# Performance work log

Measured on AMD Instinct MI355X. Metric: run time of the kernel, lower is better.

Reference implementation:

```python
import jax, jax.numpy as jnp
import numpy as np


def setup_inputs() -> dict:
    key = jax.random.key(0)
    ks = jax.random.split(key, 5)
    B, S, D = 4, 2048, 768
    scale = 0.02  # keep pre-softmax scores in a sane range
    return {
        "x": jax.random.normal(ks[0], (B, S, D), dtype=jnp.float32),
        "wq": jax.random.normal(ks[1], (D, D), dtype=jnp.float32) * scale,
        "wk": jax.random.normal(ks[2], (D, D), dtype=jnp.float32) * scale,
        "wv": jax.random.normal(ks[3], (D, D), dtype=jnp.float32) * scale,
        "wo": jax.random.normal(ks[4], (D, D), dtype=jnp.float32) * scale,
    }


NUM_HEADS = 12
NEG = -1000000000.0


def reference(x, wq, wk, wv, wo):
    B, S, D = x.shape
    H = NUM_HEADS
    dh = D // H
    # nn.Linear(bias=False): y = x @ W.T ; split heads -> [B, H, S, dh]
    def proj(w):
        return (x @ w.T).reshape(B, S, H, dh).transpose(0, 2, 1, 3)
    q, k, v = proj(wq), proj(wk), proj(wv)
    # scores [B, H, S, S] with causal mask (strict upper triangle gets -1e9 added)
    score = jnp.einsum("bhqd,bhkd->bhqk", q, k) / jnp.float32(np.sqrt(dh))
    causal = jnp.triu(jnp.ones((S, S), dtype=bool), k=1)
    score = score + jnp.where(causal, jnp.float32(NEG), jnp.float32(0.0))
    attn = jax.nn.softmax(score, axis=-1)
    out = jnp.einsum("bhqk,bhkd->bhqd", attn, v)
    out = out.transpose(0, 2, 1, 3).reshape(B, S, D)
    return out @ wo.T
```

## Files before the change

### kernel.cpp

```cpp
#include <hip/hip_runtime.h>
#include <stdint.h>

typedef unsigned short u16;
typedef __attribute__((ext_vector_type(8))) short short8;
typedef __attribute__((ext_vector_type(4))) short s16x4;
typedef __attribute__((ext_vector_type(4))) float f32x4;
typedef __attribute__((ext_vector_type(2))) unsigned uint2v;

#define MFMA16(a, b, c) __builtin_amdgcn_mfma_f32_16x16x32_bf16(a, b, c, 0, 0, 0)

#if __has_builtin(__builtin_amdgcn_mfma_f32_16x16x16bf16_1k)
__device__ __forceinline__ f32x4 pv_mfma(s16x4 a, s16x4 b, f32x4 c) {
  return __builtin_amdgcn_mfma_f32_16x16x16bf16_1k(a, b, c, 0, 0, 0);
}
#else
__device__ __forceinline__ f32x4 pv_mfma(s16x4 a, s16x4 b, f32x4 c) {
  asm volatile("v_mfma_f32_16x16x16_bf16 %0, %1, %2, %0" : "+v"(c) : "v"(a), "v"(b));
  return c;
}
#endif

__device__ __forceinline__ void async16(void* lds, const void* g) {
  __builtin_amdgcn_global_load_lds(
      (const __attribute__((address_space(1))) void*)g,
      (__attribute__((address_space(3))) void*)lds, 16, 0, 0);
}

__device__ __forceinline__ u16 f2bf(float f) {
  unsigned u = __float_as_uint(f);
  u += 0x7FFF + ((u >> 16) & 1);
  return (u16)(u >> 16);
}

__device__ __forceinline__ unsigned cvtpk(float lo, float hi) {
  unsigned r;
  asm("v_cvt_pk_bf16_f32 %0, %1, %2" : "=v"(r) : "v"(lo), "v"(hi));
  return r;
}

#define QSCALE 0.18033688011112042f
#define MASKV -30000.0f

__global__ void convert_x(const float* __restrict__ src, u16* __restrict__ dst) {
  int i = blockIdx.x * 256 + threadIdx.x;
  float4 v = ((const float4*)src)[i];
  unsigned lo = (unsigned)f2bf(v.x) | ((unsigned)f2bf(v.y) << 16);
  unsigned hi = (unsigned)f2bf(v.z) | ((unsigned)f2bf(v.w) << 16);
  ((uint2*)dst)[i] = make_uint2(lo, hi);
}

__global__ void convert_w(const float* __restrict__ wq, const float* __restrict__ wk,
                          const float* __restrict__ wv, const float* __restrict__ wo,
                          u16* __restrict__ wqkv, u16* __restrict__ wob) {
  int i = blockIdx.x * 256 + threadIdx.x;
  int wsel = i / 147456;
  int r = i - wsel * 147456;
  const float* s = (wsel == 0) ? wq : (wsel == 1) ? wk : (wsel == 2) ? wv : wo;
  float4 v = ((const float4*)s)[r];
  unsigned lo = (unsigned)f2bf(v.x) | ((unsigned)f2bf(v.y) << 16);
  unsigned hi = (unsigned)f2bf(v.z) | ((unsigned)f2bf(v.w) << 16);
  uint2 w = make_uint2(lo, hi);
  if (wsel < 3) ((uint2*)wqkv)[wsel * 147456 + r] = w;
  else ((uint2*)wob)[r] = w;
}

template <int MODE>
__global__ __launch_bounds__(256) void gemm_bt(const u16* __restrict__ A,
                                               const u16* __restrict__ Bw,
                                               u16* __restrict__ Qb, u16* __restrict__ Kb,
                                               u16* __restrict__ Vb, float* __restrict__ Out) {
  __shared__ __align__(16) u16 As[128 * 32];
  __shared__ __align__(16) u16 Bs[128 * 32];
  const int bm = blockIdx.x & 63;
  const int bn = blockIdx.x >> 6;
  const int tid = threadIdx.x;
  const int wave = tid >> 6, lane = tid & 63;
  const int arow = lane & 15, kg = lane >> 4;
  const int wr = wave >> 1, wc = wave & 1;

  const int o = tid * 16;
  const int rowS = o >> 6;
  const int cbS = o & 63;
  const char* gA0 = (const char*)A + (size_t)(bm * 128 + rowS) * 1536 + cbS;
  const char* gA1 = gA0 + (size_t)64 * 1536;
  const char* gB0 = (const char*)Bw + (size_t)(bn * 128 + rowS) * 1536 + cbS;
  const char* gB1 = gB0 + (size_t)64 * 1536;
  char* lA = (char*)As + wave * 1024;
  char* lB = (char*)Bs + wave * 1024;

  f32x4 acc[4][4];
#pragma unroll
  for (int m = 0; m < 4; ++m)
#pragma unroll
    for (int n = 0; n < 4; ++n) acc[m][n] = (f32x4)(0.0f);

  for (int kk = 0; kk < 24; ++kk) {
    async16(lA, gA0);
    async16(lA + 4096, gA1);
    async16(lB, gB0);
    async16(lB + 4096, gB1);
    gA0 += 64; gA1 += 64; gB0 += 64; gB1 += 64;
    __syncthreads();
    short8 av[4], bv[4];
#pragma unroll
    for (int m = 0; m < 4; ++m)
      av[m] = *(const short8*)(As + (wr * 64 + m * 16 + arow) * 32 + kg * 8);
#pragma unroll
    for (int n = 0; n < 4; ++n)
      bv[n] = *(const short8*)(Bs + (wc * 64 + n * 16 + arow) * 32 + kg * 8);
#pragma unroll
    for (int m = 0; m < 4; ++m)
#pragma unroll
      for (int n = 0; n < 4; ++n) acc[m][n] = MFMA16(av[m], bv[n], acc[m][n]);
    __syncthreads();
  }

#pragma unroll
  for (int m = 0; m < 4; ++m) {
    const int rbase = bm * 128 + wr * 64 + m * 16 + kg * 4;
#pragma unroll
    for (int n = 0; n < 4; ++n) {
      const int c = bn * 128 + wc * 64 + n * 16 + arow;
#pragma unroll
      for (int i = 0; i < 4; ++i) {
        float v = acc[m][n][i];
        int rr = rbase + i;
        if (MODE == 0) {
          int which = c / 768;
          int hc = c - which * 768;
          int h = hc >> 6, d = hc & 63;
          int b = rr >> 11, s = rr & 2047;
          size_t bh = (size_t)(b * 12 + h);
          if (which == 0) {
            Qb[(bh * 2048 + s) * 64 + d] = f2bf(v * QSCALE);
          } else if (which == 1) {
            Kb[(bh * 2048 + s) * 64 + d] = f2bf(v);
          } else {
            Vb[(bh * 64 + d) * 2048 + s] = f2bf(v);
          }
        } else {
          Out[(size_t)rr * 768 + c] = v;
        }
      }
    }
  }
}

__global__ __launch_bounds__(256) void attn_kernel(const u16* __restrict__ Qb,
                                                   const u16* __restrict__ Kb,
                                                   const u16* __restrict__ Vb,
                                                   u16* __restrict__ AOb) {
  __shared__ __align__(16) u16 Ks[2][64 * 64];
  __shared__ __align__(16) u16 Vt[2][64 * 64];

  const int bid = blockIdx.x;
  const int qt = 31 - (bid / 48);
  const int bh = bid % 48;
  const int tid = threadIdx.x, wave = tid >> 6, lane = tid & 63;
  const int arow = lane & 15, kg = lane >> 4;
  const size_t hbase = (size_t)bh * (2048 * 64);
  const u16* Qh = Qb + hbase;
  const int q0 = qt * 64 + wave * 16;

  short8 qf[2];
#pragma unroll
  for (int ks = 0; ks < 2; ++ks)
    qf[ks] = *(const short8*)(Qh + (size_t)(q0 + arow) * 64 + ks * 32 + kg * 8);

  f32x4 o_acc[4];
#pragma unroll
  for (int n = 0; n < 4; ++n) o_acc[n] = (f32x4)(0.0f);
  float mrow = MASKV, lrow = 0.0f;

  const int o0 = tid * 16;
  const int r0 = o0 >> 7, cb0 = o0 & 127;
  const int r1 = r0 + 32;
  const int sw0 = cb0 ^ (((r0 ^ (r0 >> 3)) & 7) << 4);
  const int sw1 = cb0 ^ (((r1 ^ (r1 >> 3)) & 7) << 4);
  char* const KsB = (char*)Ks;
  char* const VtB = (char*)Vt;
  const int ldsw = wave * 1024;

  const char* gK0 = (const char*)(Kb + hbase) + r0 * 128 + sw0;
  const char* gK1 = (const char*)(Kb + hbase) + r1 * 128 + sw1;
  const char* gV0 = (const char*)(Vb + hbase) + (size_t)r0 * 4096 + sw0;
  const char* gV1 = (const char*)(Vb + hbase) + (size_t)r1 * 4096 + sw1;

  const int ktiles = qt + 1;

  auto stage = [&](int buf) {
    async16(KsB + buf * 8192 + ldsw,        gK0);
    async16(KsB + buf * 8192 + ldsw + 4096, gK1);
    async16(VtB + buf * 8192 + ldsw,        gV0);
    async16(VtB + buf * 8192 + ldsw + 4096, gV1);
    gK0 += 8192; gK1 += 8192; gV0 += 128; gV1 += 128;
  };

  stage(0);
  asm volatile("s_waitcnt vmcnt(0)" ::: "memory");
  __builtin_amdgcn_s_barrier();

  int cur = 0;
  for (int kt = 0; kt < ktiles; ++kt) {
    if (kt + 1 < ktiles) stage(cur ^ 1);

    const char* Kc = KsB + cur * 8192;
    const char* Vc = VtB + cur * 8192;

    f32x4 s_acc[4];
#pragma unroll
    for (int cg = 0; cg < 4; ++cg) s_acc[cg] = (f32x4)(0.0f);
#pragma unroll
    for (int cg = 0; cg < 4; ++cg) {
      int krow = cg * 16 + arow;
      int fsw = ((krow ^ (krow >> 3)) & 7) << 4;
#pragma unroll
      for (int ks = 0; ks < 2; ++ks) {
        short8 kf = *(const short8*)(Kc + (krow << 7) + ((ks * 64 + kg * 16) ^ fsw));
        s_acc[cg] = MFMA16(kf, qf[ks], s_acc[cg]);
      }
    }

    if (kt == ktiles - 1) {
      int rel = wave * 16 + arow - kg * 4;
#pragma unroll
      for (int cg = 0; cg < 4; ++cg)
#pragma unroll
        for (int i = 0; i < 4; ++i)
          s_acc[cg][i] = (cg * 16 + i > rel) ? MASKV : s_acc[cg][i];
    }

    float rmax = s_acc[0][0];
#pragma unroll
    for (int cg = 0; cg < 4; ++cg)
#pragma unroll
      for (int i = 0; i < 4; ++i) rmax = fmaxf(rmax, s_acc[cg][i]);
    rmax = fmaxf(rmax, __shfl_xor(rmax, 16));
    rmax = fmaxf(rmax, __shfl_xor(rmax, 32));

    {
      float mnew = fmaxf(mrow, rmax);
      float corr = exp2f(mrow - mnew);
      mrow = mnew;
      lrow *= corr;
#pragma unroll
      for (int n = 0; n < 4; ++n)
#pragma unroll
        for (int i = 0; i < 4; ++i) o_acc[n][i] *= corr;
    }

    float p[4][4];
    float rs = 0.0f;
#pragma unroll
    for (int cg = 0; cg < 4; ++cg)
#pragma unroll
      for (int i = 0; i < 4; ++i) {
        float e = exp2f(s_acc[cg][i] - mrow);
        p[cg][i] = e;
        rs += e;
      }
    rs += __shfl_xor(rs, 16);
    rs += __shfl_xor(rs, 32);
    lrow += rs;

    s16x4 pb[4];
#pragma unroll
    for (int cg = 0; cg < 4; ++cg) {
      uint2v w;
      w.x = cvtpk(p[cg][0], p[cg][1]);
      w.y = cvtpk(p[cg][2], p[cg][3]);
      pb[cg] = __builtin_bit_cast(s16x4, w);
    }

#pragma unroll
    for (int n = 0; n < 4; ++n) {
      int vrow = n * 16 + arow;
      int f2 = ((vrow ^ (vrow >> 3)) & 7) << 4;
      const char* vb0 = Vc + (vrow << 7);
#pragma unroll
      for (int cg = 0; cg < 4; ++cg) {
        s16x4 va = *(const s16x4*)(vb0 + ((cg * 32 + kg * 8) ^ f2));
        o_acc[n] = pv_mfma(va, pb[cg], o_acc[n]);
      }
    }

    asm volatile("s_waitcnt vmcnt(0)" ::: "memory");
    __builtin_amdgcn_s_barrier();
    cur ^= 1;
  }

  const int b = bh / 12, h = bh - b * 12;
  float rinv = 1.0f / lrow;
  size_t obase = ((size_t)b * 2048 + q0 + arow) * 768 + h * 64 + kg * 4;
#pragma unroll
  for (int n = 0; n < 4; ++n) {
#pragma unroll
    for (int t = 0; t < 2; ++t) {
      unsigned w = cvtpk(o_acc[n][2 * t] * rinv, o_acc[n][2 * t + 1] * rinv);
      *(unsigned*)(&AOb[obase + n * 16 + 2 * t]) = w;
    }
  }
}

extern "C" void kernel_launch(void* const* d_in, const int* in_sizes, int n_in,
                              void* d_out, int out_size, void* d_ws, size_t ws_size,
                              hipStream_t stream) {
  const float* x = (const float*)d_in[0];
  const float* wq = (const float*)d_in[1];
  const float* wk = (const float*)d_in[2];
  const float* wv = (const float*)d_in[3];
  const float* wo = (const float*)d_in[4];
  float* out = (float*)d_out;

  char* ws = (char*)d_ws;
  u16* xb   = (u16*)(ws);
  u16* wqkv = (u16*)(ws + 12582912);
  u16* wob  = (u16*)(ws + 16121856);
  u16* Qb   = (u16*)(ws + 17301504);
  u16* Kb   = (u16*)(ws + 29884416);
  u16* Vb   = (u16*)(ws + 42467328);
  u16* AOb  = (u16*)(ws + 55050240);

  convert_x<<<6144, 256, 0, stream>>>(x, xb);
  convert_w<<<2304, 256, 0, stream>>>(wq, wk, wv, wo, wqkv, wob);

  gemm_bt<0><<<64 * 18, 256, 0, stream>>>(xb, wqkv, Qb, Kb, Vb, nullptr);
  attn_kernel<<<48 * 32, 256, 0, stream>>>(Qb, Kb, Vb, AOb);
  gemm_bt<1><<<64 * 6, 256, 0, stream>>>(AOb, wob, nullptr, nullptr, nullptr, out);
}
```

Before: 153.1 us.

## Double-buffer GEMM LDS tiles and vectorize the transposed V epilogue stores

The QKV and output GEMMs now use two LDS buffers, so the async global-to-LDS load of the next K-slice is issued before the MFMAs on the current slice run. This overlaps memory latency with compute and leaves one barrier per iteration instead of two. The epilogue is also restructured: per-block values (head, which matrix) are hoisted, and the transposed V output is packed two bf16 at a time into 8-byte stores instead of scattered scalar writes. The cost is doubled LDS per block, which may reduce occupancy, and a vmcnt(0) wait that still stalls on each stage.

```diff
diff --git a/kernel.cpp b/kernel.cpp
--- a/kernel.cpp
+++ b/kernel.cpp
@@ -69,8 +69,8 @@
                                                const u16* __restrict__ Bw,
                                                u16* __restrict__ Qb, u16* __restrict__ Kb,
                                                u16* __restrict__ Vb, float* __restrict__ Out) {
-  __shared__ __align__(16) u16 As[128 * 32];
-  __shared__ __align__(16) u16 Bs[128 * 32];
+  __shared__ __align__(16) u16 As[2][128 * 32];
+  __shared__ __align__(16) u16 Bs[2][128 * 32];
   const int bm = blockIdx.x & 63;
   const int bn = blockIdx.x >> 6;
   const int tid = threadIdx.x;
@@ -85,8 +85,7 @@
   const char* gA1 = gA0 + (size_t)64 * 1536;
   const char* gB0 = (const char*)Bw + (size_t)(bn * 128 + rowS) * 1536 + cbS;
   const char* gB1 = gB0 + (size_t)64 * 1536;
-  char* lA = (char*)As + wave * 1024;
-  char* lB = (char*)Bs + wave * 1024;
+  const int ldsw = wave * 1024;
 
   f32x4 acc[4][4];
 #pragma unroll
@@ -94,55 +93,84 @@
 #pragma unroll
     for (int n = 0; n < 4; ++n) acc[m][n] = (f32x4)(0.0f);
 
+  auto stage = [&](int buf) {
+    async16((char*)As + buf * 8192 + ldsw,        gA0);
+    async16((char*)As + buf * 8192 + ldsw + 4096, gA1);
+    async16((char*)Bs + buf * 8192 + ldsw,        gB0);
+    async16((char*)Bs + buf * 8192 + ldsw + 4096, gB1);
+    gA0 += 64; gA1 += 64; gB0 += 64; gB1 += 64;
+  };
+
+  stage(0);
+  asm volatile("s_waitcnt vmcnt(0)" ::: "memory");
+  __builtin_amdgcn_s_barrier();
+
+  int cur = 0;
   for (int kk = 0; kk < 24; ++kk) {
-    async16(lA, gA0);
-    async16(lA + 4096, gA1);
-    async16(lB, gB0);
-    async16(lB + 4096, gB1);
-    gA0 += 64; gA1 += 64; gB0 += 64; gB1 += 64;
-    __syncthreads();
+    if (kk + 1 < 24) stage(cur ^ 1);
+
+    const char* Ac = (const char*)As + cur * 8192;
+    const char* Bc = (const char*)Bs + cur * 8192;
     short8 av[4], bv[4];
 #pragma unroll
     for (int m = 0; m < 4; ++m)
-      av[m] = *(const short8*)(As + (wr * 64 + m * 16 + arow) * 32 + kg * 8);
+      av[m] = *(const short8*)(Ac + (wr * 64 + m * 16 + arow) * 64 + kg * 16);
 #pragma unroll
     for (int n = 0; n < 4; ++n)
-      bv[n] = *(const short8*)(Bs + (wc * 64 + n * 16 + arow) * 32 + kg * 8);
+      bv[n] = *(const short8*)(Bc + (wc * 64 + n * 16 + arow) * 64 + kg * 16);
 #pragma unroll
     for (int m = 0; m < 4; ++m)
 #pragma unroll
       for (int n = 0; n < 4; ++n) acc[m][n] = MFMA16(av[m], bv[n], acc[m][n]);
-    __syncthreads();
+
+    asm volatile("s_waitcnt vmcnt(0)" ::: "memory");
+    __builtin_amdgcn_s_barrier();
+    cur ^= 1;
   }
 
-#pragma unroll
-  for (int m = 0; m < 4; ++m) {
-    const int rbase = bm * 128 + wr * 64 + m * 16 + kg * 4;
-#pragma unroll
-    for (int n = 0; n < 4; ++n) {
-      const int c = bn * 128 + wc * 64 + n * 16 + arow;
-#pragma unroll
-      for (int i = 0; i < 4; ++i) {
-        float v = acc[m][n][i];
-        int rr = rbase + i;
-        if (MODE == 0) {
-          int which = c / 768;
-          int hc = c - which * 768;
-          int h = hc >> 6, d = hc & 63;
-          int b = rr >> 11, s = rr & 2047;
-          size_t bh = (size_t)(b * 12 + h);
-          if (which == 0) {
-            Qb[(bh * 2048 + s) * 64 + d] = f2bf(v * QSCALE);
-          } else if (which == 1) {
-            Kb[(bh * 2048 + s) * 64 + d] = f2bf(v);
-          } else {
-            Vb[(bh * 64 + d) * 2048 + s] = f2bf(v);
-          }
-        } else {
-          Out[(size_t)rr * 768 + c] = v;
+  if (MODE == 0) {
+    const int b = bm >> 4;
+    const int sb = (bm & 15) * 128 + wr * 64 + kg * 4;
+    const int which = bn / 6;
+    const int cbase = bn * 128 - which * 768 + wc * 64;
+    if (which == 2) {
+#pragma unroll
+      for (int n = 0; n < 4; ++n) {
+        int hc = cbase + n * 16 + arow;
+        size_t rowb = ((size_t)(b * 12 + (hc >> 6)) * 64 + (hc & 63)) * 2048;
+#pragma unroll
+        for (int m = 0; m < 4; ++m) {
+          uint2v w;
+          w.x = cvtpk(acc[m][n][0], acc[m][n][1]);
+          w.y = cvtpk(acc[m][n][2], acc[m][n][3]);
+          *(uint2v*)(Vb + rowb + sb + m * 16) = w;
         }
       }
-    }
+    } else {
+      u16* const dst = which ? Kb : Qb;
+      const float sc = which ? 1.0f : QSCALE;
+#pragma unroll
+      for (int n = 0; n < 4; ++n) {
+        int hc = cbase + n * 16 + arow;
+        size_t hb = ((size_t)(b * 12 + (hc >> 6)) * 2048) * 64 + (hc & 63);
+#pragma unroll
+        for (int m = 0; m < 4; ++m)
+#pragma unroll
+          for (int i = 0; i < 4; ++i)
+            dst[hb + (size_t)(sb + m * 16 + i) * 64] = f2bf(acc[m][n][i] * sc);
+      }
+    }
+  } else {
+    const int rbase = bm * 128 + wr * 64 + kg * 4;
+#pragma unroll
+    for (int m = 0; m < 4; ++m)
+#pragma unroll
+      for (int n = 0; n < 4; ++n) {
+        const int c = bn * 128 + wc * 64 + n * 16 + arow;
+#pragma unroll
+        for (int i = 0; i < 4; ++i)
+          Out[(size_t)(rbase + m * 16 + i) * 768 + c] = acc[m][n][i];
+      }
   }
 }
 
```

After: 140.6 us. -8.2%, faster.
